# Optimization experiments

Hardware: AMD Instinct MI355X
Metric: run time of the kernel (lower is better)

## Reference

```python
import jax, jax.numpy as jnp
import numpy as np

IN_DIM, HIDDEN_DIM, OUT_DIM = 128, 64, 64
N_NODES, N_EDGES = 100000, 1000000


def gcn_layer(x, src, dst, W, b):
    """PyG GCNConv: h = W x; out = D^-1/2 (A+I) D^-1/2 h + b (self-loops already in src/dst)."""
    n = x.shape[0]
    deg = jax.ops.segment_sum(jnp.ones_like(src, dtype=x.dtype), dst, num_segments=n)
    dinv = jnp.where(deg > 0, jax.lax.rsqrt(deg), 0.0)
    norm = dinv[src] * dinv[dst]          # [E+N]
    h = x @ W                              # [N, out]
    msg = h[src] * norm[:, None]           # [E+N, out] gather + scale
    out = jax.ops.segment_sum(msg, dst, num_segments=n)  # scatter-add
    return out + b


def setup_inputs() -> dict:
    key = jax.random.key(0)
    k1, k2, k3, k4 = jax.random.split(key, 4)
    x = jax.random.normal(k1, (N_NODES, IN_DIM), dtype=jnp.float32)
    edge_index = jax.random.randint(k2, (2, N_EDGES), 0, N_NODES, dtype=jnp.int64)
    # Glorot-ish init for the two GCNConv linear weights; zero biases (PyG default)
    W1 = jax.random.normal(k3, (IN_DIM, HIDDEN_DIM), dtype=jnp.float32) / np.sqrt(IN_DIM)
    W2 = jax.random.normal(k4, (HIDDEN_DIM, OUT_DIM), dtype=jnp.float32) / np.sqrt(HIDDEN_DIM)
    b1 = jnp.zeros((HIDDEN_DIM,), dtype=jnp.float32)
    b2 = jnp.zeros((OUT_DIM,), dtype=jnp.float32)
    return {"x": x, "edge_index": edge_index, "W1": W1, "b1": b1, "W2": W2, "b2": b2}


def reference(x, edge_index, W1, b1, W2, b2):
    n = x.shape[0]
    loops = jnp.arange(n, dtype=edge_index.dtype)
    src = jnp.concatenate([edge_index[0], loops])  # add self-loops once
    dst = jnp.concatenate([edge_index[1], loops])
    x1 = gcn_layer(x, src, dst, W1, b1)
    h = jax.nn.relu(x1)
    # dropout is identity in eval/reference mode
    x2 = gcn_layer(h, src, dst, W2, b2)
    return x2
```

## Files before the change

### kernel.cpp

```cpp
#include <hip/hip_runtime.h>
#include <hip/hip_fp16.h>

#define DIM_IN 128
#define DIM_HID 64
#define BK_SHIFT 9
#define BK_SIZE 512
#define SRC_BITS 17
#define CAP 6144
#define CAP2 8192
#define P_EPT  16
#define P_TILE 4096

typedef _Float16 half8 __attribute__((ext_vector_type(8)));
typedef float floatx4 __attribute__((ext_vector_type(4)));


__global__ void zero_kernel(int* __restrict__ bcur, float* __restrict__ dinv_sent) {
    bcur[threadIdx.x] = 0;
    if (threadIdx.x == 0) dinv_sent[0] = 0.0f;
}


__global__ __launch_bounds__(256)
void gemm1_partition_kernel(const float* __restrict__ x, const float* __restrict__ W,
                            _Float16* __restrict__ h, int n, int gb,
                            const int* __restrict__ src, const int* __restrict__ dst,
                            int* __restrict__ bcur, int* __restrict__ part, int E) {
    __shared__ int smem[5888];
    const int tid = threadIdx.x;

    if (blockIdx.x < gb) {
        constexpr int K = DIM_IN, LDK = K + 8;
        _Float16* Wt = (_Float16*)smem;
        for (int idx = tid; idx < K * 64; idx += 256) {
            int k = idx >> 6, c = idx & 63;
            Wt[c * LDK + k] = (_Float16)W[idx];
        }
        __syncthreads();

        const int wave = tid >> 6;
        const int lane = tid & 63;
        const int r    = lane & 15;
        const int g    = lane >> 4;
        const int row0 = blockIdx.x * 64 + wave * 16;
        const int arow = row0 + r;
        const float* xrow = x + (size_t)(arow < n ? arow : 0) * K + g * 8;

        floatx4 acc0 = {}, acc1 = {}, acc2 = {}, acc3 = {};
#pragma unroll
        for (int kt = 0; kt < K / 32; ++kt) {
            float4 a0 = *(const float4*)(xrow + kt * 32);
            float4 a1 = *(const float4*)(xrow + kt * 32 + 4);
            half8 a;
            a[0] = (_Float16)a0.x; a[1] = (_Float16)a0.y;
            a[2] = (_Float16)a0.z; a[3] = (_Float16)a0.w;
            a[4] = (_Float16)a1.x; a[5] = (_Float16)a1.y;
            a[6] = (_Float16)a1.z; a[7] = (_Float16)a1.w;

            const _Float16* wb = &Wt[r * LDK + kt * 32 + g * 8];
            half8 b0 = *(const half8*)(wb + 0 * 16 * LDK);
            half8 b1 = *(const half8*)(wb + 1 * 16 * LDK);
            half8 b2 = *(const half8*)(wb + 2 * 16 * LDK);
            half8 b3 = *(const half8*)(wb + 3 * 16 * LDK);
            acc0 = __builtin_amdgcn_mfma_f32_16x16x32_f16(a, b0, acc0, 0, 0, 0);
            acc1 = __builtin_amdgcn_mfma_f32_16x16x32_f16(a, b1, acc1, 0, 0, 0);
            acc2 = __builtin_amdgcn_mfma_f32_16x16x32_f16(a, b2, acc2, 0, 0, 0);
            acc3 = __builtin_amdgcn_mfma_f32_16x16x32_f16(a, b3, acc3, 0, 0, 0);
        }

#pragma unroll
        for (int j = 0; j < 4; ++j) {
            int drow = row0 + g * 4 + j;
            _Float16* o = h + (size_t)drow * 64 + r;
            if (drow < n) {
                o[0]  = (_Float16)acc0[j];
                o[16] = (_Float16)acc1[j];
                o[32] = (_Float16)acc2[j];
                o[48] = (_Float16)acc3[j];
            } else {
                o[0] = (_Float16)0; o[16] = (_Float16)0;
                o[32] = (_Float16)0; o[48] = (_Float16)0;
            }
        }
    } else {
        int* hist  = smem;
        int* bofs  = smem + 256;
        int* gbase = smem + 512;
        int* stage = smem + 768;
        unsigned char* auxb = (unsigned char*)(smem + 4864);
        const int tile0 = (blockIdx.x - gb) * P_TILE;
        const int tcnt  = min(P_TILE, E - tile0);

        hist[tid] = 0;
        __syncthreads();

        int pack[P_EPT], bb[P_EPT], lo[P_EPT];
#pragma unroll
        for (int i = 0; i < P_EPT; ++i) {
            int e = tile0 + i * 256 + tid;
            bb[i] = -1;
            if (e < E) {
                int d = dst[e];
                int s = src[e];
                bb[i]   = d >> BK_SHIFT;
                pack[i] = ((d & (BK_SIZE - 1)) << SRC_BITS) | s;
                lo[i]   = atomicAdd(&hist[bb[i]], 1);
            }
        }
        __syncthreads();

        bofs[tid] = hist[tid];
        __syncthreads();
        for (int off = 1; off < 256; off <<= 1) {
            int t = (tid >= off) ? bofs[tid - off] : 0;
            __syncthreads();
            bofs[tid] += t;
            __syncthreads();
        }
        int ex = bofs[tid] - hist[tid];
        __syncthreads();
        bofs[tid] = ex;
        if (hist[tid]) gbase[tid] = tid * CAP + atomicAdd(&bcur[tid], hist[tid]);
        __syncthreads();

#pragma unroll
        for (int i = 0; i < P_EPT; ++i) {
            if (bb[i] >= 0) {
                int p = bofs[bb[i]] + lo[i];
                stage[p] = pack[i];
                auxb[p]  = (unsigned char)bb[i];
            }
        }
        __syncthreads();

        for (int k = tid; k < tcnt; k += 256) {
            int b = auxb[k];
            part[gbase[b] + (k - bofs[b])] = stage[k];
        }
    }
}


__global__ __launch_bounds__(256)
void bucket_fill_kernel(const int* __restrict__ bcur, const int* __restrict__ part,
                        int2* __restrict__ nodeinfo, float* __restrict__ dinv,
                        int* __restrict__ srcs, int n, int zrow) {
    __shared__ int cnt[BK_SIZE];
    __shared__ int rp[BK_SIZE];
    __shared__ int s2[256];
    __shared__ int total;
    const int tid   = threadIdx.x;
    const int bid   = blockIdx.x;
    const int node0 = bid << BK_SHIFT;
    const int bs    = min(BK_SIZE, n - node0);
    const int pbase = bid * CAP;
    const int sbase = bid * CAP2;
    const int ecnt  = bcur[bid];

    cnt[tid] = 0; cnt[tid + 256] = 0;
    __syncthreads();
    for (int k = tid; k < ecnt; k += 256)
        atomicAdd(&cnt[part[pbase + k] >> SRC_BITS], 1);
    __syncthreads();

    int c0 = cnt[2 * tid], c1 = cnt[2 * tid + 1];
    int p0 = (c0 + 3) & ~3, p1 = (c1 + 3) & ~3;
    s2[tid] = p0 + p1;
    __syncthreads();
    for (int off = 1; off < 256; off <<= 1) {
        int t = (tid >= off) ? s2[tid - off] : 0;
        __syncthreads();
        s2[tid] += t;
        __syncthreads();
    }
    int ex = s2[tid] - (p0 + p1);
    rp[2 * tid]     = ex;
    rp[2 * tid + 1] = ex + p0;
    if (tid == 255) total = s2[255];
    __syncthreads();

    for (int i = tid; i < bs; i += 256) {
        int c = cnt[i];
        nodeinfo[node0 + i] = make_int2(sbase + rp[i], (c + 3) & ~3);
        dinv[node0 + i]     = rsqrtf((float)c + 1.0f);
    }
    __syncthreads();

    cnt[tid] = 0; cnt[tid + 256] = 0;
    for (int k = tid; k < total; k += 256) srcs[sbase + k] = zrow;
    __syncthreads();
    for (int k = tid; k < ecnt; k += 256) {
        int v    = part[pbase + k];
        int li   = v >> SRC_BITS;
        int slot = atomicAdd(&cnt[li], 1);
        srcs[sbase + rp[li] + slot] = v & ((1 << SRC_BITS) - 1);
    }
}


__global__ __launch_bounds__(256)
void layer2_fused_kernel(const int2* __restrict__ nodeinfo, const int* __restrict__ srcs,
                         const float* __restrict__ dinv, const half8* __restrict__ hs,
                         const float* __restrict__ b1, const float* __restrict__ W2,
                         _Float16* __restrict__ h2, int n) {
    __shared__ _Float16 At[64 * 72];
    __shared__ _Float16 Wt[64 * 72];
    const int tid = threadIdx.x;

    for (int idx = tid; idx < 64 * 64; idx += 256) {
        int k = idx >> 6, c = idx & 63;
        Wt[c * 72 + k] = (_Float16)W2[idx];
    }

    const int f    = tid & 7;
    const int grp  = tid >> 3;
    const int row0 = blockIdx.x * 64;

#pragma unroll
    for (int rnd = 0; rnd < 2; ++rnd) {
        const int nrow = rnd * 32 + grp;
        const int node = row0 + nrow;
        half8 o = {};
        if (node < n) {
            int2 info = nodeinfo[node];
            int start = info.x, cpad = info.y;
            float dn = dinv[node];
            half8 sv = hs[(size_t)node * 8 + f];
            float acc[8];
#pragma unroll
            for (int i = 0; i < 8; ++i) acc[i] = dn * (float)sv[i];

            for (int j = 0; j < cpad; j += 4) {
                int4 ss = *(const int4*)&srcs[start + j];
                float d0 = dinv[ss.x], d1 = dinv[ss.y], d2 = dinv[ss.z], d3 = dinv[ss.w];
                half8 v0 = hs[(size_t)ss.x * 8 + f];
                half8 v1 = hs[(size_t)ss.y * 8 + f];
                half8 v2 = hs[(size_t)ss.z * 8 + f];
                half8 v3 = hs[(size_t)ss.w * 8 + f];
#pragma unroll
                for (int i = 0; i < 8; ++i)
                    acc[i] += (d0 * (float)v0[i] + d1 * (float)v1[i]) +
                              (d2 * (float)v2[i] + d3 * (float)v3[i]);
            }
#pragma unroll
            for (int i = 0; i < 8; ++i) {
                float g1 = fmaf(acc[i], dn, b1[f * 8 + i]);
                o[i] = (_Float16)fmaxf(g1, 0.0f);
            }
        }
        *(half8*)&At[nrow * 72 + f * 8] = o;
    }
    __syncthreads();

    const int wave = tid >> 6;
    const int lane = tid & 63;
    const int r    = lane & 15;
    const int g    = lane >> 4;

    floatx4 acc0 = {}, acc1 = {}, acc2 = {}, acc3 = {};
#pragma unroll
    for (int kt = 0; kt < 2; ++kt) {
        half8 a = *(const half8*)&At[(wave * 16 + r) * 72 + kt * 32 + g * 8];
        const _Float16* wb = &Wt[r * 72 + kt * 32 + g * 8];
        half8 b0 = *(const half8*)(wb + 0 * 16 * 72);
        half8 b1v = *(const half8*)(wb + 1 * 16 * 72);
        half8 b2v = *(const half8*)(wb + 2 * 16 * 72);
        half8 b3v = *(const half8*)(wb + 3 * 16 * 72);
        acc0 = __builtin_amdgcn_mfma_f32_16x16x32_f16(a, b0, acc0, 0, 0, 0);
        acc1 = __builtin_amdgcn_mfma_f32_16x16x32_f16(a, b1v, acc1, 0, 0, 0);
        acc2 = __builtin_amdgcn_mfma_f32_16x16x32_f16(a, b2v, acc2, 0, 0, 0);
        acc3 = __builtin_amdgcn_mfma_f32_16x16x32_f16(a, b3v, acc3, 0, 0, 0);
    }

#pragma unroll
    for (int j = 0; j < 4; ++j) {
        int drow = row0 + wave * 16 + g * 4 + j;
        _Float16* o = h2 + (size_t)drow * 64 + r;
        o[0]  = (_Float16)acc0[j];
        o[16] = (_Float16)acc1[j];
        o[32] = (_Float16)acc2[j];
        o[48] = (_Float16)acc3[j];
    }
}


__global__ __launch_bounds__(256)
void gather_out_kernel(const int2* __restrict__ nodeinfo, const int* __restrict__ srcs,
                       const float* __restrict__ dinv, const half8* __restrict__ hs,
                       const float* __restrict__ b, float* __restrict__ out, int n) {
    const int tid  = threadIdx.x;
    const int f    = tid & 7;
    const int node = blockIdx.x * 32 + (tid >> 3);
    if (node >= n) return;

    int2 info = nodeinfo[node];
    int start = info.x, cpad = info.y;
    float dn = dinv[node];

    half8 sv = hs[(size_t)node * 8 + f];
    float acc[8];
#pragma unroll
    for (int i = 0; i < 8; ++i) acc[i] = dn * (float)sv[i];

    for (int j = 0; j < cpad; j += 4) {
        int4 ss = *(const int4*)&srcs[start + j];
        float d0 = dinv[ss.x], d1 = dinv[ss.y], d2 = dinv[ss.z], d3 = dinv[ss.w];
        half8 v0 = hs[(size_t)ss.x * 8 + f];
        half8 v1 = hs[(size_t)ss.y * 8 + f];
        half8 v2 = hs[(size_t)ss.z * 8 + f];
        half8 v3 = hs[(size_t)ss.w * 8 + f];
#pragma unroll
        for (int i = 0; i < 8; ++i)
            acc[i] += (d0 * (float)v0[i] + d1 * (float)v1[i]) +
                      (d2 * (float)v2[i] + d3 * (float)v3[i]);
    }

    const float4* b4 = (const float4*)b;
    float4 bb0 = b4[f * 2], bb1 = b4[f * 2 + 1];
    float4 o0 = make_float4(fmaf(acc[0], dn, bb0.x), fmaf(acc[1], dn, bb0.y),
                            fmaf(acc[2], dn, bb0.z), fmaf(acc[3], dn, bb0.w));
    float4 o1 = make_float4(fmaf(acc[4], dn, bb1.x), fmaf(acc[5], dn, bb1.y),
                            fmaf(acc[6], dn, bb1.z), fmaf(acc[7], dn, bb1.w));
    float4* o4 = (float4*)out;
    o4[(size_t)node * 16 + f * 2]     = o0;
    o4[(size_t)node * 16 + f * 2 + 1] = o1;
}


extern "C" void kernel_launch(void* const* d_in, const int* in_sizes, int n_in,
                              void* d_out, int out_size, void* d_ws, size_t ws_size,
                              hipStream_t stream) {
    const float* x   = (const float*)d_in[0];
    const int*   ei  = (const int*)d_in[1];
    const float* W1  = (const float*)d_in[2];
    const float* b1  = (const float*)d_in[3];
    const float* W2  = (const float*)d_in[4];
    const float* b2  = (const float*)d_in[5];
    float*       out = (float*)d_out;

    const int n = in_sizes[0] / DIM_IN;
    const int E = in_sizes[1] / 2;
    const int* srcp = ei;
    const int* dstp = ei + E;
    const int NB    = (n + BK_SIZE - 1) >> BK_SHIFT;
    const int gb    = (n + 63) / 64;
    const int pb    = (E + P_TILE - 1) / P_TILE;
    const int ab    = (n + 31) / 32;
    const size_t nrows = (size_t)gb * 64;

    const int npad = ((n + 255) / 256) * 256;

    int*      bcur     = (int*)d_ws;
    int2*     nodeinfo = (int2*)(bcur + 256);
    float*    dinv     = (float*)((int*)nodeinfo + 2 * npad);
    int*      srcs     = (int*)(dinv + npad);
    int*      part     = srcs + (size_t)NB * CAP2;
    _Float16* h        = (_Float16*)(part + (size_t)NB * CAP);
    _Float16* h2       = h + nrows * 64;

    zero_kernel<<<1, 256, 0, stream>>>(bcur, &dinv[n]);
    gemm1_partition_kernel<<<gb + pb, 256, 0, stream>>>(x, W1, h, n, gb,
                                                        srcp, dstp, bcur, part, E);
    bucket_fill_kernel<<<NB, 256, 0, stream>>>(bcur, part, nodeinfo, dinv, srcs, n, n);
    layer2_fused_kernel<<<gb, 256, 0, stream>>>(nodeinfo, srcs, dinv, (const half8*)h,
                                                b1, W2, h2, n);
    gather_out_kernel<<<ab, 256, 0, stream>>>(nodeinfo, srcs, dinv, (const half8*)h2,
                                              b2, out, n);
}
```

Measured before the change: 102.1 us.

## Degree-sort nodes within buckets and pre-scale layer-2 features by dinv

The bucket fill kernel now builds a per-bucket permutation that groups nodes by padded in-degree. Both gather kernels walk nodes in that order, so the threads of a wave have similar loop trip counts and less divergence. Layer-2 features are also written pre-multiplied by the source node's dinv, which removes the per-edge dinv loads and multiplies in the final gather. The cost is an extra indirection through the order array, scattered row writes in the layer-2 epilogue, and zeroing of a padding row used as the sentinel source.

```diff
diff --git a/kernel.cpp b/kernel.cpp
--- a/kernel.cpp
+++ b/kernel.cpp
@@ -15,9 +15,11 @@
 typedef float floatx4 __attribute__((ext_vector_type(4)));
 
 
-__global__ void zero_kernel(int* __restrict__ bcur, float* __restrict__ dinv_sent) {
+__global__ void zero_kernel(int* __restrict__ bcur, float* __restrict__ dinv_sent,
+                            int* __restrict__ h2row_n) {
     bcur[threadIdx.x] = 0;
     if (threadIdx.x == 0) dinv_sent[0] = 0.0f;
+    if (threadIdx.x < 32) h2row_n[threadIdx.x] = 0;
 }
 
 
@@ -144,10 +146,12 @@
 __global__ __launch_bounds__(256)
 void bucket_fill_kernel(const int* __restrict__ bcur, const int* __restrict__ part,
                         int2* __restrict__ nodeinfo, float* __restrict__ dinv,
-                        int* __restrict__ srcs, int n, int zrow) {
+                        int* __restrict__ srcs, int* __restrict__ order,
+                        int n, int zrow) {
     __shared__ int cnt[BK_SIZE];
     __shared__ int rp[BK_SIZE];
     __shared__ int s2[256];
+    __shared__ int hist2[32];
     __shared__ int total;
     const int tid   = threadIdx.x;
     const int bid   = blockIdx.x;
@@ -158,6 +162,7 @@
     const int ecnt  = bcur[bid];
 
     cnt[tid] = 0; cnt[tid + 256] = 0;
+    if (tid < 32) hist2[tid] = 0;
     __syncthreads();
     for (int k = tid; k < ecnt; k += 256)
         atomicAdd(&cnt[part[pbase + k] >> SRC_BITS], 1);
@@ -183,10 +188,24 @@
         int c = cnt[i];
         nodeinfo[node0 + i] = make_int2(sbase + rp[i], (c + 3) & ~3);
         dinv[node0 + i]     = rsqrtf((float)c + 1.0f);
+        atomicAdd(&hist2[min((c + 3) >> 2, 31)], 1);
+    }
+    __syncthreads();
+
+    if (tid == 0) {
+        int run = 0;
+        for (int b = 0; b < 32; ++b) { int t = hist2[b]; hist2[b] = run; run += t; }
+    }
+    __syncthreads();
+    for (int i = tid; i < bs; i += 256) {
+        int k = min((cnt[i] + 3) >> 2, 31);
+        int pos = atomicAdd(&hist2[k], 1);
+        order[node0 + pos] = node0 + i;
     }
     __syncthreads();
 
     cnt[tid] = 0; cnt[tid + 256] = 0;
+    __syncthreads();
     for (int k = tid; k < total; k += 256) srcs[sbase + k] = zrow;
     __syncthreads();
     for (int k = tid; k < ecnt; k += 256) {
@@ -200,9 +219,9 @@
 
 __global__ __launch_bounds__(256)
 void layer2_fused_kernel(const int2* __restrict__ nodeinfo, const int* __restrict__ srcs,
-                         const float* __restrict__ dinv, const half8* __restrict__ hs,
-                         const float* __restrict__ b1, const float* __restrict__ W2,
-                         _Float16* __restrict__ h2, int n) {
+                         const float* __restrict__ dinv, const int* __restrict__ order,
+                         const half8* __restrict__ hs, const float* __restrict__ b1,
+                         const float* __restrict__ W2, _Float16* __restrict__ h2, int n) {
     __shared__ _Float16 At[64 * 72];
     __shared__ _Float16 Wt[64 * 72];
     const int tid = threadIdx.x;
@@ -219,9 +238,9 @@
 #pragma unroll
     for (int rnd = 0; rnd < 2; ++rnd) {
         const int nrow = rnd * 32 + grp;
-        const int node = row0 + nrow;
         half8 o = {};
-        if (node < n) {
+        if (row0 + nrow < n) {
+            const int node = order[row0 + nrow];
             int2 info = nodeinfo[node];
             int start = info.x, cpad = info.y;
             float dn = dinv[node];
@@ -274,47 +293,51 @@
 
 #pragma unroll
     for (int j = 0; j < 4; ++j) {
-        int drow = row0 + wave * 16 + g * 4 + j;
-        _Float16* o = h2 + (size_t)drow * 64 + r;
-        o[0]  = (_Float16)acc0[j];
-        o[16] = (_Float16)acc1[j];
-        o[32] = (_Float16)acc2[j];
-        o[48] = (_Float16)acc3[j];
+        int rl = row0 + wave * 16 + g * 4 + j;
+        if (rl < n) {
+            int node2 = order[rl];
+            float dn2 = dinv[node2];
+            _Float16* o = h2 + (size_t)node2 * 64 + r;
+            o[0]  = (_Float16)(acc0[j] * dn2);
+            o[16] = (_Float16)(acc1[j] * dn2);
+            o[32] = (_Float16)(acc2[j] * dn2);
+            o[48] = (_Float16)(acc3[j] * dn2);
+        }
     }
 }
 
 
 __global__ __launch_bounds__(256)
 void gather_out_kernel(const int2* __restrict__ nodeinfo, const int* __restrict__ srcs,
-                       const float* __restrict__ dinv, const half8* __restrict__ hs,
-                       const float* __restrict__ b, float* __restrict__ out, int n) {
+                       const float* __restrict__ dinv, const int* __restrict__ order,
+                       const half8* __restrict__ hs, const float* __restrict__ b,
+                       float* __restrict__ out, int n) {
     const int tid  = threadIdx.x;
     const int f    = tid & 7;
-    const int node = blockIdx.x * 32 + (tid >> 3);
-    if (node >= n) return;
+    const int gidx = blockIdx.x * 32 + (tid >> 3);
+    if (gidx >= n) return;
+    const int node = order[gidx];
 
     int2 info = nodeinfo[node];
     int start = info.x, cpad = info.y;
-    float dn = dinv[node];
 
     half8 sv = hs[(size_t)node * 8 + f];
     float acc[8];
 #pragma unroll
-    for (int i = 0; i < 8; ++i) acc[i] = dn * (float)sv[i];
+    for (int i = 0; i < 8; ++i) acc[i] = (float)sv[i];
 
     for (int j = 0; j < cpad; j += 4) {
         int4 ss = *(const int4*)&srcs[start + j];
-        float d0 = dinv[ss.x], d1 = dinv[ss.y], d2 = dinv[ss.z], d3 = dinv[ss.w];
         half8 v0 = hs[(size_t)ss.x * 8 + f];
         half8 v1 = hs[(size_t)ss.y * 8 + f];
         half8 v2 = hs[(size_t)ss.z * 8 + f];
         half8 v3 = hs[(size_t)ss.w * 8 + f];
 #pragma unroll
         for (int i = 0; i < 8; ++i)
-            acc[i] += (d0 * (float)v0[i] + d1 * (float)v1[i]) +
-                      (d2 * (float)v2[i] + d3 * (float)v3[i]);
-    }
-
+            acc[i] += ((float)v0[i] + (float)v1[i]) + ((float)v2[i] + (float)v3[i]);
+    }
+
+    float dn = dinv[node];
     const float4* b4 = (const float4*)b;
     float4 bb0 = b4[f * 2], bb1 = b4[f * 2 + 1];
     float4 o0 = make_float4(fmaf(acc[0], dn, bb0.x), fmaf(acc[1], dn, bb0.y),
@@ -353,17 +376,18 @@
     int*      bcur     = (int*)d_ws;
     int2*     nodeinfo = (int2*)(bcur + 256);
     float*    dinv     = (float*)((int*)nodeinfo + 2 * npad);
-    int*      srcs     = (int*)(dinv + npad);
+    int*      order    = (int*)(dinv + npad);
+    int*      srcs     = order + npad;
     int*      part     = srcs + (size_t)NB * CAP2;
     _Float16* h        = (_Float16*)(part + (size_t)NB * CAP);
     _Float16* h2       = h + nrows * 64;
 
-    zero_kernel<<<1, 256, 0, stream>>>(bcur, &dinv[n]);
+    zero_kernel<<<1, 256, 0, stream>>>(bcur, &dinv[n], (int*)(h2 + (size_t)n * 64));
     gemm1_partition_kernel<<<gb + pb, 256, 0, stream>>>(x, W1, h, n, gb,
                                                         srcp, dstp, bcur, part, E);
-    bucket_fill_kernel<<<NB, 256, 0, stream>>>(bcur, part, nodeinfo, dinv, srcs, n, n);
-    layer2_fused_kernel<<<gb, 256, 0, stream>>>(nodeinfo, srcs, dinv, (const half8*)h,
+    bucket_fill_kernel<<<NB, 256, 0, stream>>>(bcur, part, nodeinfo, dinv, srcs, order, n, n);
+    layer2_fused_kernel<<<gb, 256, 0, stream>>>(nodeinfo, srcs, dinv, order, (const half8*)h,
                                                 b1, W2, h2, n);
-    gather_out_kernel<<<ab, 256, 0, stream>>>(nodeinfo, srcs, dinv, (const half8*)h2,
+    gather_out_kernel<<<ab, 256, 0, stream>>>(nodeinfo, srcs, dinv, order, (const half8*)h2,
                                               b2, out, n);
 }
```

Measured after the change: 113.3 us. 1.11x slower.
